# Kernel tuning notes

Measured on AMD Instinct MI355X. Metric: run time of the kernel, lower is better.

## Reference

```python
import jax, jax.numpy as jnp
import numpy as np

D = 2048
N_HEAD = 16
D_HEAD = D // N_HEAD
EXP = 4
EPS = 1e-6


def setup_inputs() -> dict:
    key = jax.random.key(0)
    ks = jax.random.split(key, 8)
    b, s = 2, 2048
    scale = 0.02
    return {
        "x": jax.random.normal(ks[0], (b, s, D), dtype=jnp.float32),
        "w_qkv": jax.random.normal(ks[1], (D, 3 * D), dtype=jnp.float32) * scale,
        "w_o": jax.random.normal(ks[2], (D, D), dtype=jnp.float32) * scale,
        "w_up": jax.random.normal(ks[3], (D, EXP * D), dtype=jnp.float32) * scale,
        "w_gate": jax.random.normal(ks[4], (D, EXP * D), dtype=jnp.float32) * scale,
        "w_down": jax.random.normal(ks[5], (EXP * D, D), dtype=jnp.float32) * scale,
        "scale1": jnp.ones((D,), dtype=jnp.float32),
        "scale2": jnp.ones((D,), dtype=jnp.float32),
    }


def _rmsnorm(x, scale):
    rms = jnp.sqrt(jnp.mean(x * x, axis=-1, keepdims=True) + EPS)
    return x / rms * scale


def _attention(x, w_qkv, w_o):
    b, s, d = x.shape
    qkv = x @ w_qkv  # [b, s, 3d]
    q, k, v = jnp.split(qkv, 3, axis=-1)
    # [b, h, s, dh]
    q = q.reshape(b, s, N_HEAD, D_HEAD).transpose(0, 2, 1, 3)
    k = k.reshape(b, s, N_HEAD, D_HEAD).transpose(0, 2, 1, 3)
    v = v.reshape(b, s, N_HEAD, D_HEAD).transpose(0, 2, 1, 3)
    scores = jnp.einsum("bhqd,bhkd->bhqk", q, k) / np.sqrt(D_HEAD).astype(np.float32)
    causal = jnp.tril(jnp.ones((s, s), dtype=bool))
    scores = jnp.where(causal, scores, -jnp.inf)
    attn = jax.nn.softmax(scores, axis=-1)
    out = jnp.einsum("bhqk,bhkd->bhqd", attn, v)
    out = out.transpose(0, 2, 1, 3).reshape(b, s, d)
    return out @ w_o


def _mlp(x, w_up, w_gate, w_down):
    return (x @ w_up * jax.nn.silu(x @ w_gate)) @ w_down


def reference(x, w_qkv, w_o, w_up, w_gate, w_down, scale1, scale2):
    x = x + _attention(_rmsnorm(x, scale1), w_qkv, w_o)
    x = x + _mlp(_rmsnorm(x, scale2), w_up, w_gate, w_down)
    return x
```

## Files before the change

### kernel.cpp

```cpp
#include <hip/hip_runtime.h>

typedef unsigned short u16;
typedef __bf16 bfrag8 __attribute__((ext_vector_type(8)));
typedef float f32x4 __attribute__((ext_vector_type(4)));

#define MFMA16(a, b, c) __builtin_amdgcn_mfma_f32_16x16x32_bf16((a), (b), (c), 0, 0, 0)

static __device__ __forceinline__ u16 bf_bits(float f) {
  unsigned int u = __builtin_bit_cast(unsigned int, f);
  unsigned int r = (u + 0x7fffu + ((u >> 16) & 1u)) >> 16;
  return (u16)r;
}
static __device__ __forceinline__ float f_from_bits(u16 u) {
  unsigned int w = ((unsigned int)u) << 16;
  return __builtin_bit_cast(float, w);
}
static __device__ __forceinline__ void gload16(const void* g, void* l) {
  __builtin_amdgcn_global_load_lds(
      (const __attribute__((address_space(1))) void*)g,
      (__attribute__((address_space(3))) void*)l, 16, 0, 0);
}

__global__ __launch_bounds__(256) void k_transpose_bf16(const float* __restrict__ src,
                                                        u16* __restrict__ dst,
                                                        int K, int N) {
  __shared__ float tile[32][33];
  const int n0 = blockIdx.x * 32;
  const int k0 = blockIdx.y * 32;
  const int t = threadIdx.x;
  const int lr = t >> 5;
  const int lc = t & 31;
#pragma unroll
  for (int i = 0; i < 4; ++i)
    tile[lr + i * 8][lc] = src[(size_t)(k0 + lr + i * 8) * N + n0 + lc];
  __syncthreads();
#pragma unroll
  for (int i = 0; i < 4; ++i)
    dst[(size_t)(n0 + lr + i * 8) * K + k0 + lc] = bf_bits(tile[lc][lr + i * 8]);
}

__global__ __launch_bounds__(256) void k_transpose_v(const u16* __restrict__ qkv,
                                                     u16* __restrict__ vtg) {
  __shared__ u16 tile[32][33];
  const int bh = blockIdx.z, b = bh >> 4, hh = bh & 15;
  const int s0 = blockIdx.x * 32, d0 = blockIdx.y * 32;
  const int t = threadIdx.x;
  const int lr = t >> 5, lc = t & 31;
#pragma unroll
  for (int i = 0; i < 4; ++i)
    tile[lr + i * 8][lc] =
        qkv[(size_t)(b * 2048 + s0 + lr + i * 8) * 6144 + 4096 + hh * 128 + d0 + lc];
  __syncthreads();
#pragma unroll
  for (int i = 0; i < 4; ++i)
    vtg[(size_t)bh * 128 * 2048 + (size_t)(d0 + lr + i * 8) * 2048 + s0 + lc] =
        tile[lc][lr + i * 8];
}

__global__ __launch_bounds__(256) void k_rmsnorm(const float* __restrict__ x,
                                                 const float* __restrict__ sc,
                                                 u16* __restrict__ o) {
  const int row = blockIdx.x;
  const int t = threadIdx.x;
  const float4* x4 = (const float4*)(x + (size_t)row * 2048);
  float4 a = x4[t];
  float4 b = x4[t + 256];
  float ss = a.x * a.x + a.y * a.y + a.z * a.z + a.w * a.w +
             b.x * b.x + b.y * b.y + b.z * b.z + b.w * b.w;
#pragma unroll
  for (int off = 32; off > 0; off >>= 1) ss += __shfl_down(ss, off);
  __shared__ float red[4];
  if ((t & 63) == 0) red[t >> 6] = ss;
  __syncthreads();
  const float inv = rsqrtf((red[0] + red[1] + red[2] + red[3]) * (1.0f / 2048.0f) + 1e-6f);
  const float4* s4 = (const float4*)sc;
  float4 sa = s4[t], sb = s4[t + 256];
  ushort4 pa, pb;
  pa.x = bf_bits(a.x * inv * sa.x); pa.y = bf_bits(a.y * inv * sa.y);
  pa.z = bf_bits(a.z * inv * sa.z); pa.w = bf_bits(a.w * inv * sa.w);
  pb.x = bf_bits(b.x * inv * sb.x); pb.y = bf_bits(b.y * inv * sb.y);
  pb.z = bf_bits(b.z * inv * sb.z); pb.w = bf_bits(b.w * inv * sb.w);
  *(ushort4*)(o + (size_t)row * 2048 + t * 4) = pa;
  *(ushort4*)(o + (size_t)row * 2048 + (t + 256) * 4) = pb;
}

template <int EPI, int K, int PART>
__global__ __launch_bounds__(256, 4) void k_gemm(const u16* __restrict__ A,
                                                 const u16* __restrict__ Bt,
                                                 int M, int N,
                                                 float* __restrict__ outF,
                                                 u16* __restrict__ outB,
                                                 const float* __restrict__ resid,
                                                 const u16* __restrict__ gate) {
  __shared__ u16 sm[16384];
  char* smC = (char*)sm;
  const int nbx = gridDim.x;
  const int f = blockIdx.x + nbx * blockIdx.y;
  int m0, n0;
  if (PART == 0) {
    const int nsl = nbx >> 3;
    const int x = f & 7;
    const int j = f >> 3;
    n0 = (x * nsl + (j % nsl)) * 128;
    m0 = (j / nsl) * 128;
  } else {
    const int msl = (int)gridDim.y >> 3;
    const int x = f & 7;
    const int j = f >> 3;
    m0 = (x * msl + (j % msl)) * 128;
    n0 = (j / msl) * 128;
  }

  const int t = threadIdx.x;
  const int wid = t >> 6, lane = t & 63;
  const int wm = wid >> 1, wn = wid & 1;
  const int l15 = lane & 15, lhi = lane >> 4;
  const int lhi16 = lhi * 16;
  const int swz = (l15 & 7) << 4;

  f32x4 acc[4][4];
#pragma unroll
  for (int i = 0; i < 4; ++i)
#pragma unroll
    for (int j2 = 0; j2 < 4; ++j2) acc[i][j2] = (f32x4){0.f, 0.f, 0.f, 0.f};

  const int sr = lane >> 3;
  const int csw = (((lane & 7) * 16) ^ (sr << 4)) >> 1;
  const u16* Asrc = A + (size_t)(m0 + wid * 32 + sr) * K + csw;
  const u16* Bsrc = Bt + (size_t)(n0 + wid * 32 + sr) * K + csw;
  char* adst = smC + wid * 4096 + lane * 16;
  char* bdst = smC + 16384 + wid * 4096 + lane * 16;

  for (int kt = 0; kt < K / 64; ++kt) {
    __syncthreads();
    const u16* as = Asrc + kt * 64;
    const u16* bs = Bsrc + kt * 64;
#pragma unroll
    for (int c = 0; c < 4; ++c) {
      gload16(as + (size_t)c * 8 * K, adst + c * 1024);
      gload16(bs + (size_t)c * 8 * K, bdst + c * 1024);
    }
    asm volatile("s_waitcnt vmcnt(0)" ::: "memory");
    __syncthreads();

#pragma unroll
    for (int kh = 0; kh < 2; ++kh) {
      const int ko = kh * 64 + lhi16;
      bfrag8 a0 = *(const bfrag8*)(smC + (wm * 64 + 0 * 16 + l15) * 128 + (ko ^ swz));
      bfrag8 a1 = *(const bfrag8*)(smC + (wm * 64 + 1 * 16 + l15) * 128 + (ko ^ swz));
      bfrag8 a2 = *(const bfrag8*)(smC + (wm * 64 + 2 * 16 + l15) * 128 + (ko ^ swz));
      bfrag8 a3 = *(const bfrag8*)(smC + (wm * 64 + 3 * 16 + l15) * 128 + (ko ^ swz));
      bfrag8 b0 = *(const bfrag8*)(smC + 16384 + (wn * 64 + 0 * 16 + l15) * 128 + (ko ^ swz));
      bfrag8 b1 = *(const bfrag8*)(smC + 16384 + (wn * 64 + 1 * 16 + l15) * 128 + (ko ^ swz));
      bfrag8 b2 = *(const bfrag8*)(smC + 16384 + (wn * 64 + 2 * 16 + l15) * 128 + (ko ^ swz));
      bfrag8 b3 = *(const bfrag8*)(smC + 16384 + (wn * 64 + 3 * 16 + l15) * 128 + (ko ^ swz));
      acc[0][0] = MFMA16(a0, b0, acc[0][0]); acc[0][1] = MFMA16(a0, b1, acc[0][1]);
      acc[0][2] = MFMA16(a0, b2, acc[0][2]); acc[0][3] = MFMA16(a0, b3, acc[0][3]);
      acc[1][0] = MFMA16(a1, b0, acc[1][0]); acc[1][1] = MFMA16(a1, b1, acc[1][1]);
      acc[1][2] = MFMA16(a1, b2, acc[1][2]); acc[1][3] = MFMA16(a1, b3, acc[1][3]);
      acc[2][0] = MFMA16(a2, b0, acc[2][0]); acc[2][1] = MFMA16(a2, b1, acc[2][1]);
      acc[2][2] = MFMA16(a2, b2, acc[2][2]); acc[2][3] = MFMA16(a2, b3, acc[2][3]);
      acc[3][0] = MFMA16(a3, b0, acc[3][0]); acc[3][1] = MFMA16(a3, b1, acc[3][1]);
      acc[3][2] = MFMA16(a3, b2, acc[3][2]); acc[3][3] = MFMA16(a3, b3, acc[3][3]);
    }
  }

#pragma unroll
  for (int i = 0; i < 4; ++i) {
#pragma unroll
    for (int j2 = 0; j2 < 4; ++j2) {
      const int mr = m0 + wm * 64 + i * 16 + lhi * 4;
      const int nc = n0 + wn * 64 + j2 * 16 + l15;
#pragma unroll
      for (int r = 0; r < 4; ++r) {
        const size_t idx = (size_t)(mr + r) * N + nc;
        const float v = acc[i][j2][r];
        if (EPI == 0) {
          outB[idx] = bf_bits(v);
        } else if (EPI == 1) {
          outF[idx] = resid[idx] + v;
        } else {
          float g = f_from_bits(gate[idx]);
          float s = g / (1.f + __expf(-g));
          outB[idx] = bf_bits(v * s);
        }
      }
    }
  }
}

template <int EPI, int K, int PART>
__global__ __launch_bounds__(256, 3) void k_gemm2(const u16* __restrict__ A,
                                                  const u16* __restrict__ Bt,
                                                  int N,
                                                  float* __restrict__ outF,
                                                  u16* __restrict__ outB,
                                                  const float* __restrict__ resid) {
  __shared__ u16 sm[24576];
  char* smC = (char*)sm;
  const int nbx = gridDim.x;
  const int f = blockIdx.x + nbx * blockIdx.y;
  int m0, np;
  if (PART == 0) {
    const int nsl = nbx >> 3;
    const int x = f & 7;
    const int j = f >> 3;
    np = x * nsl + (j % nsl);
    m0 = (j / nsl) * 128;
  } else {
    const int msl = (int)gridDim.y >> 3;
    const int x = f & 7;
    const int j = f >> 3;
    m0 = (x * msl + (j % msl)) * 128;
    np = j / msl;
  }
  const int n0 = np * 256;

  const int t = threadIdx.x;
  const int wid = t >> 6, lane = t & 63;
  const int wm = wid >> 1, wn = wid & 1;
  const int l15 = lane & 15, lhi = lane >> 4;
  const int lhi16 = lhi * 16;
  const int swz = (l15 & 7) << 4;

  f32x4 acc0[4][4], acc1[4][4];
#pragma unroll
  for (int i = 0; i < 4; ++i)
#pragma unroll
    for (int j2 = 0; j2 < 4; ++j2) {
      acc0[i][j2] = (f32x4){0.f, 0.f, 0.f, 0.f};
      acc1[i][j2] = (f32x4){0.f, 0.f, 0.f, 0.f};
    }

  const int sr = lane >> 3;
  const int csw = (((lane & 7) * 16) ^ (sr << 4)) >> 1;
  const u16* Asrc = A + (size_t)(m0 + wid * 32 + sr) * K + csw;
  const u16* B0src = Bt + (size_t)(n0 + wid * 32 + sr) * K + csw;
  const u16* B1src = Bt + (size_t)(n0 + 128 + wid * 32 + sr) * K + csw;
  char* adst = smC + wid * 4096 + lane * 16;
  char* b0dst = smC + 16384 + wid * 4096 + lane * 16;
  char* b1dst = smC + 32768 + wid * 4096 + lane * 16;

  for (int kt = 0; kt < K / 64; ++kt) {
    __syncthreads();
    const u16* as = Asrc + kt * 64;
    const u16* b0s = B0src + kt * 64;
    const u16* b1s = B1src + kt * 64;
#pragma unroll
    for (int c = 0; c < 4; ++c) {
      gload16(as + (size_t)c * 8 * K, adst + c * 1024);
      gload16(b0s + (size_t)c * 8 * K, b0dst + c * 1024);
      gload16(b1s + (size_t)c * 8 * K, b1dst + c * 1024);
    }
    asm volatile("s_waitcnt vmcnt(0)" ::: "memory");
    __syncthreads();

#pragma unroll
    for (int kh = 0; kh < 2; ++kh) {
      const int ko = (kh * 64 + lhi16);
      bfrag8 a0 = *(const bfrag8*)(smC + (wm * 64 + 0 * 16 + l15) * 128 + (ko ^ swz));
      bfrag8 a1 = *(const bfrag8*)(smC + (wm * 64 + 1 * 16 + l15) * 128 + (ko ^ swz));
      bfrag8 a2 = *(const bfrag8*)(smC + (wm * 64 + 2 * 16 + l15) * 128 + (ko ^ swz));
      bfrag8 a3 = *(const bfrag8*)(smC + (wm * 64 + 3 * 16 + l15) * 128 + (ko ^ swz));
      bfrag8 g0 = *(const bfrag8*)(smC + 16384 + (wn * 64 + 0 * 16 + l15) * 128 + (ko ^ swz));
      bfrag8 g1 = *(const bfrag8*)(smC + 16384 + (wn * 64 + 1 * 16 + l15) * 128 + (ko ^ swz));
      bfrag8 g2 = *(const bfrag8*)(smC + 16384 + (wn * 64 + 2 * 16 + l15) * 128 + (ko ^ swz));
      bfrag8 g3 = *(const bfrag8*)(smC + 16384 + (wn * 64 + 3 * 16 + l15) * 128 + (ko ^ swz));
      acc0[0][0] = MFMA16(a0, g0, acc0[0][0]); acc0[0][1] = MFMA16(a0, g1, acc0[0][1]);
      acc0[0][2] = MFMA16(a0, g2, acc0[0][2]); acc0[0][3] = MFMA16(a0, g3, acc0[0][3]);
      acc0[1][0] = MFMA16(a1, g0, acc0[1][0]); acc0[1][1] = MFMA16(a1, g1, acc0[1][1]);
      acc0[1][2] = MFMA16(a1, g2, acc0[1][2]); acc0[1][3] = MFMA16(a1, g3, acc0[1][3]);
      acc0[2][0] = MFMA16(a2, g0, acc0[2][0]); acc0[2][1] = MFMA16(a2, g1, acc0[2][1]);
      acc0[2][2] = MFMA16(a2, g2, acc0[2][2]); acc0[2][3] = MFMA16(a2, g3, acc0[2][3]);
      acc0[3][0] = MFMA16(a3, g0, acc0[3][0]); acc0[3][1] = MFMA16(a3, g1, acc0[3][1]);
      acc0[3][2] = MFMA16(a3, g2, acc0[3][2]); acc0[3][3] = MFMA16(a3, g3, acc0[3][3]);
      bfrag8 u0 = *(const bfrag8*)(smC + 32768 + (wn * 64 + 0 * 16 + l15) * 128 + (ko ^ swz));
      bfrag8 u1 = *(const bfrag8*)(smC + 32768 + (wn * 64 + 1 * 16 + l15) * 128 + (ko ^ swz));
      bfrag8 u2 = *(const bfrag8*)(smC + 32768 + (wn * 64 + 2 * 16 + l15) * 128 + (ko ^ swz));
      bfrag8 u3 = *(const bfrag8*)(smC + 32768 + (wn * 64 + 3 * 16 + l15) * 128 + (ko ^ swz));
      acc1[0][0] = MFMA16(a0, u0, acc1[0][0]); acc1[0][1] = MFMA16(a0, u1, acc1[0][1]);
      acc1[0][2] = MFMA16(a0, u2, acc1[0][2]); acc1[0][3] = MFMA16(a0, u3, acc1[0][3]);
      acc1[1][0] = MFMA16(a1, u0, acc1[1][0]); acc1[1][1] = MFMA16(a1, u1, acc1[1][1]);
      acc1[1][2] = MFMA16(a1, u2, acc1[1][2]); acc1[1][3] = MFMA16(a1, u3, acc1[1][3]);
      acc1[2][0] = MFMA16(a2, u0, acc1[2][0]); acc1[2][1] = MFMA16(a2, u1, acc1[2][1]);
      acc1[2][2] = MFMA16(a2, u2, acc1[2][2]); acc1[2][3] = MFMA16(a2, u3, acc1[2][3]);
      acc1[3][0] = MFMA16(a3, u0, acc1[3][0]); acc1[3][1] = MFMA16(a3, u1, acc1[3][1]);
      acc1[3][2] = MFMA16(a3, u2, acc1[3][2]); acc1[3][3] = MFMA16(a3, u3, acc1[3][3]);
    }
  }

#pragma unroll
  for (int h = 0; h < 2; ++h) {
#pragma unroll
    for (int i = 0; i < 4; ++i) {
#pragma unroll
      for (int j2 = 0; j2 < 4; ++j2) {
        const int mr = m0 + wm * 64 + i * 16 + lhi * 4;
        const int nc = n0 + h * 128 + wn * 64 + j2 * 16 + l15;
#pragma unroll
        for (int r = 0; r < 4; ++r) {
          const size_t idx = (size_t)(mr + r) * N + nc;
          const float v = h ? acc1[i][j2][r] : acc0[i][j2][r];
          if (EPI == 0) {
            outB[idx] = bf_bits(v);
          } else {
            outF[idx] = resid[idx] + v;
          }
        }
      }
    }
  }
}

template <int K>
__global__ __launch_bounds__(256, 3) void k_gemm_mlp(const u16* __restrict__ A,
                                                     const u16* __restrict__ Bg,
                                                     const u16* __restrict__ Bu,
                                                     int N,
                                                     u16* __restrict__ outB) {
  __shared__ u16 sm[24576];
  char* smC = (char*)sm;
  const int nbx = gridDim.x;
  const int f = blockIdx.x + nbx * blockIdx.y;
  const int nsl = nbx >> 3;
  const int x = f & 7;
  const int j = f >> 3;
  const int n0 = (x * nsl + (j % nsl)) * 128;
  const int m0 = (j / nsl) * 128;

  const int t = threadIdx.x;
  const int wid = t >> 6, lane = t & 63;
  const int wm = wid >> 1, wn = wid & 1;
  const int l15 = lane & 15, lhi = lane >> 4;
  const int lhi16 = lhi * 16;
  const int swz = (l15 & 7) << 4;

  f32x4 accg[4][4], accu[4][4];
#pragma unroll
  for (int i = 0; i < 4; ++i)
#pragma unroll
    for (int j2 = 0; j2 < 4; ++j2) {
      accg[i][j2] = (f32x4){0.f, 0.f, 0.f, 0.f};
      accu[i][j2] = (f32x4){0.f, 0.f, 0.f, 0.f};
    }

  const int sr = lane >> 3;
  const int csw = (((lane & 7) * 16) ^ (sr << 4)) >> 1;
  const u16* Asrc = A + (size_t)(m0 + wid * 32 + sr) * K + csw;
  const u16* Bgsrc = Bg + (size_t)(n0 + wid * 32 + sr) * K + csw;
  const u16* Busrc = Bu + (size_t)(n0 + wid * 32 + sr) * K + csw;
  char* adst = smC + wid * 4096 + lane * 16;
  char* bgdst = smC + 16384 + wid * 4096 + lane * 16;
  char* budst = smC + 32768 + wid * 4096 + lane * 16;

  for (int kt = 0; kt < K / 64; ++kt) {
    __syncthreads();
    const u16* as = Asrc + kt * 64;
    const u16* gs = Bgsrc + kt * 64;
    const u16* us = Busrc + kt * 64;
#pragma unroll
    for (int c = 0; c < 4; ++c) {
      gload16(as + (size_t)c * 8 * K, adst + c * 1024);
      gload16(gs + (size_t)c * 8 * K, bgdst + c * 1024);
      gload16(us + (size_t)c * 8 * K, budst + c * 1024);
    }
    asm volatile("s_waitcnt vmcnt(0)" ::: "memory");
    __syncthreads();

#pragma unroll
    for (int kh = 0; kh < 2; ++kh) {
      const int ko = (kh * 64 + lhi16);
      bfrag8 a0 = *(const bfrag8*)(smC + (wm * 64 + 0 * 16 + l15) * 128 + (ko ^ swz));
      bfrag8 a1 = *(const bfrag8*)(smC + (wm * 64 + 1 * 16 + l15) * 128 + (ko ^ swz));
      bfrag8 a2 = *(const bfrag8*)(smC + (wm * 64 + 2 * 16 + l15) * 128 + (ko ^ swz));
      bfrag8 a3 = *(const bfrag8*)(smC + (wm * 64 + 3 * 16 + l15) * 128 + (ko ^ swz));
      bfrag8 g0 = *(const bfrag8*)(smC + 16384 + (wn * 64 + 0 * 16 + l15) * 128 + (ko ^ swz));
      bfrag8 g1 = *(const bfrag8*)(smC + 16384 + (wn * 64 + 1 * 16 + l15) * 128 + (ko ^ swz));
      bfrag8 g2 = *(const bfrag8*)(smC + 16384 + (wn * 64 + 2 * 16 + l15) * 128 + (ko ^ swz));
      bfrag8 g3 = *(const bfrag8*)(smC + 16384 + (wn * 64 + 3 * 16 + l15) * 128 + (ko ^ swz));
      accg[0][0] = MFMA16(a0, g0, accg[0][0]); accg[0][1] = MFMA16(a0, g1, accg[0][1]);
      accg[0][2] = MFMA16(a0, g2, accg[0][2]); accg[0][3] = MFMA16(a0, g3, accg[0][3]);
      accg[1][0] = MFMA16(a1, g0, accg[1][0]); accg[1][1] = MFMA16(a1, g1, accg[1][1]);
      accg[1][2] = MFMA16(a1, g2, accg[1][2]); accg[1][3] = MFMA16(a1, g3, accg[1][3]);
      accg[2][0] = MFMA16(a2, g0, accg[2][0]); accg[2][1] = MFMA16(a2, g1, accg[2][1]);
      accg[2][2] = MFMA16(a2, g2, accg[2][2]); accg[2][3] = MFMA16(a2, g3, accg[2][3]);
      accg[3][0] = MFMA16(a3, g0, accg[3][0]); accg[3][1] = MFMA16(a3, g1, accg[3][1]);
      accg[3][2] = MFMA16(a3, g2, accg[3][2]); accg[3][3] = MFMA16(a3, g3, accg[3][3]);
      bfrag8 u0 = *(const bfrag8*)(smC + 32768 + (wn * 64 + 0 * 16 + l15) * 128 + (ko ^ swz));
      bfrag8 u1 = *(const bfrag8*)(smC + 32768 + (wn * 64 + 1 * 16 + l15) * 128 + (ko ^ swz));
      bfrag8 u2 = *(const bfrag8*)(smC + 32768 + (wn * 64 + 2 * 16 + l15) * 128 + (ko ^ swz));
      bfrag8 u3 = *(const bfrag8*)(smC + 32768 + (wn * 64 + 3 * 16 + l15) * 128 + (ko ^ swz));
      accu[0][0] = MFMA16(a0, u0, accu[0][0]); accu[0][1] = MFMA16(a0, u1, accu[0][1]);
      accu[0][2] = MFMA16(a0, u2, accu[0][2]); accu[0][3] = MFMA16(a0, u3, accu[0][3]);
      accu[1][0] = MFMA16(a1, u0, accu[1][0]); accu[1][1] = MFMA16(a1, u1, accu[1][1]);
      accu[1][2] = MFMA16(a1, u2, accu[1][2]); accu[1][3] = MFMA16(a1, u3, accu[1][3]);
      accu[2][0] = MFMA16(a2, u0, accu[2][0]); accu[2][1] = MFMA16(a2, u1, accu[2][1]);
      accu[2][2] = MFMA16(a2, u2, accu[2][2]); accu[2][3] = MFMA16(a2, u3, accu[2][3]);
      accu[3][0] = MFMA16(a3, u0, accu[3][0]); accu[3][1] = MFMA16(a3, u1, accu[3][1]);
      accu[3][2] = MFMA16(a3, u2, accu[3][2]); accu[3][3] = MFMA16(a3, u3, accu[3][3]);
    }
  }

#pragma unroll
  for (int i = 0; i < 4; ++i) {
#pragma unroll
    for (int j2 = 0; j2 < 4; ++j2) {
      const int mr = m0 + wm * 64 + i * 16 + lhi * 4;
      const int nc = n0 + wn * 64 + j2 * 16 + l15;
#pragma unroll
      for (int r = 0; r < 4; ++r) {
        const float g = accg[i][j2][r];
        const float u = accu[i][j2][r];
        const float s = g / (1.f + __expf(-g));
        outB[(size_t)(mr + r) * N + nc] = bf_bits(u * s);
      }
    }
  }
}

__global__ __launch_bounds__(512) void k_attn(const u16* __restrict__ qkv,
                                              const u16* __restrict__ vtg,
                                              u16* __restrict__ out) {
  const int S = 2048, LD = 6144;
  const float scale = 0.0883883476483184405f;
  const int fid = blockIdx.x;
  const int p = fid >> 1, s = fid & 1;
  const int bh = p & 31;
  const int pq = p >> 5;
  const int qt = s ? (15 - pq) : pq;
  const int b = bh >> 4, hh = bh & 15;
  const int t = threadIdx.x;
  const int wave = t >> 6, lane = t & 63;
  const int l15 = lane & 15, lhi = lane >> 4;
  const int lhi16 = lhi * 16;
  const int swz = (l15 & 7) << 4;

  __shared__ u16 Kt[64 * 128];
  __shared__ u16 Vt[128 * 64];
  __shared__ u16 Pl[8][16][72];
  char* KtC = (char*)Kt;
  char* VtC = (char*)Vt;

  const int qrow = qt * 128 + wave * 16 + l15;
  const size_t qoff = (size_t)(b * S + qrow) * LD + hh * 128 + lhi * 8;
  bfrag8 qf[4];
#pragma unroll
  for (int ks = 0; ks < 4; ++ks) qf[ks] = *(const bfrag8*)(qkv + qoff + ks * 32);

  f32x4 oacc[8];
#pragma unroll
  for (int j = 0; j < 8; ++j) oacc[j] = (f32x4){0.f, 0.f, 0.f, 0.f};
  float m_i[4], l_i[4];
#pragma unroll
  for (int r = 0; r < 4; ++r) { m_i[r] = -INFINITY; l_i[r] = 0.f; }

  const int q_my = qt * 128 + wave * 16 + lhi * 4;
  const int q_wave_last = qt * 128 + wave * 16 + 15;

  const int keyA = t >> 4, keyB = 32 + (t >> 4);
  const int oK = (t & 15) * 16;
  const int dA = t >> 3, dB = 64 + (t >> 3);
  const int oV = (t & 7) * 16;
  const u16* kbase = qkv + (size_t)(b * S) * LD + 2048 + hh * 128;
  const u16* vbase = vtg + (size_t)bh * 128 * S;
  const u16* ksrcA = kbase + (size_t)keyA * LD + ((oK ^ ((keyA & 7) << 4)) >> 1);
  const u16* ksrcB = kbase + (size_t)keyB * LD + ((oK ^ ((keyB & 7) << 4)) >> 1);
  const u16* vsrcA = vbase + (size_t)dA * S + ((oV ^ ((dA & 7) << 4)) >> 1);
  const u16* vsrcB = vbase + (size_t)dB * S + ((oV ^ ((dB & 7) << 4)) >> 1);
  const unsigned int ldso0 = wave * 1024 + lane * 16;
  const unsigned int ldso1 = 8192 + wave * 1024 + lane * 16;
  const size_t kstep = (size_t)64 * LD;

  const int kt_max = 2 * qt + 1;
  for (int kt = 0; kt <= kt_max; ++kt) {
    __syncthreads();
    gload16(ksrcA + (size_t)kt * kstep, KtC + ldso0);
    gload16(ksrcB + (size_t)kt * kstep, KtC + ldso1);
    gload16(vsrcA + kt * 64, VtC + ldso0);
    gload16(vsrcB + kt * 64, VtC + ldso1);
    __syncthreads();

    if (kt * 64 <= q_wave_last) {
      f32x4 sfr[4];
#pragma unroll
      for (int j = 0; j < 4; ++j) {
        sfr[j] = (f32x4){0.f, 0.f, 0.f, 0.f};
        const int krow = j * 16 + l15;
#pragma unroll
        for (int ks = 0; ks < 4; ++ks) {
          bfrag8 kf = *(const bfrag8*)(KtC + krow * 256 + ((ks * 64 + lhi16) ^ swz));
          sfr[j] = MFMA16(qf[ks], kf, sfr[j]);
        }
      }
      float sv[4][4], rmax[4];
#pragma unroll
      for (int r = 0; r < 4; ++r) rmax[r] = -INFINITY;
#pragma unroll
      for (int j = 0; j < 4; ++j) {
        const int key = kt * 64 + j * 16 + l15;
#pragma unroll
        for (int r = 0; r < 4; ++r) {
          float v = sfr[j][r] * scale;
          v = (key <= q_my + r) ? v : -INFINITY;
          sv[j][r] = v;
          rmax[r] = fmaxf(rmax[r], v);
        }
      }
#pragma unroll
      for (int r = 0; r < 4; ++r) {
        float v = rmax[r];
        v = fmaxf(v, __shfl_xor(v, 1));
        v = fmaxf(v, __shfl_xor(v, 2));
        v = fmaxf(v, __shfl_xor(v, 4));
        v = fmaxf(v, __shfl_xor(v, 8));
        rmax[r] = v;
      }
      float alpha[4], rsum[4];
#pragma unroll
      for (int r = 0; r < 4; ++r) {
        float mn = fmaxf(m_i[r], rmax[r]);
        alpha[r] = __expf(m_i[r] - mn);
        m_i[r] = mn;
        rsum[r] = 0.f;
      }
#pragma unroll
      for (int j = 0; j < 4; ++j) {
#pragma unroll
        for (int r = 0; r < 4; ++r) {
          float p2 = __expf(sv[j][r] - m_i[r]);
          rsum[r] += p2;
          Pl[wave][lhi * 4 + r][j * 16 + l15] = bf_bits(p2);
        }
      }
#pragma unroll
      for (int r = 0; r < 4; ++r) {
        float v = rsum[r];
        v += __shfl_xor(v, 1); v += __shfl_xor(v, 2);
        v += __shfl_xor(v, 4); v += __shfl_xor(v, 8);
        l_i[r] = l_i[r] * alpha[r] + v;
      }
#pragma unroll
      for (int j = 0; j < 8; ++j)
#pragma unroll
        for (int r = 0; r < 4; ++r) oacc[j][r] *= alpha[r];

#pragma unroll
      for (int ks2 = 0; ks2 < 2; ++ks2) {
        bfrag8 pf = *(const bfrag8*)&Pl[wave][l15][ks2 * 32 + lhi * 8];
#pragma unroll
        for (int j = 0; j < 8; ++j) {
          const int d = j * 16 + l15;
          bfrag8 vf = *(const bfrag8*)(VtC + d * 128 + ((ks2 * 64 + lhi16) ^ swz));
          oacc[j] = MFMA16(pf, vf, oacc[j]);
        }
      }
    }
  }

#pragma unroll
  for (int r = 0; r < 4; ++r) {
    const float inv = 1.f / l_i[r];
    const size_t tok = (size_t)b * S + qt * 128 + wave * 16 + lhi * 4 + r;
#pragma unroll
    for (int j = 0; j < 8; ++j)
      out[tok * 2048 + hh * 128 + j * 16 + l15] = bf_bits(oacc[j][r] * inv);
  }
}

extern "C" void kernel_launch(void* const* d_in, const int* in_sizes, int n_in,
                              void* d_out, int out_size, void* d_ws, size_t ws_size,
                              hipStream_t stream) {
  (void)in_sizes; (void)n_in; (void)out_size; (void)ws_size;
  const float* x      = (const float*)d_in[0];
  const float* w_qkv  = (const float*)d_in[1];
  const float* w_o    = (const float*)d_in[2];
  const float* w_up   = (const float*)d_in[3];
  const float* w_gate = (const float*)d_in[4];
  const float* w_down = (const float*)d_in[5];
  const float* scale1 = (const float*)d_in[6];
  const float* scale2 = (const float*)d_in[7];
  float* out = (float*)d_out;

  u16* B       = (u16*)d_ws;
  u16* wqkvT   = B;
  u16* woT     = wqkvT  + (size_t)6144 * 2048;
  u16* wgateT  = woT    + (size_t)2048 * 2048;
  u16* wupT    = wgateT + (size_t)8192 * 2048;
  u16* wdownT  = wupT   + (size_t)8192 * 2048;
  u16* xn      = wdownT + (size_t)2048 * 8192;
  u16* qkvb    = xn     + (size_t)4096 * 2048;
  u16* attnb   = qkvb   + (size_t)4096 * 6144;
  float* y1    = (float*)(attnb + (size_t)4096 * 2048);
  u16* vtg     = (u16*)y1;
  u16* hbuf    = qkvb;

  dim3 blk(256);
  k_transpose_bf16<<<dim3(192, 64), blk, 0, stream>>>(w_qkv,  wqkvT,  2048, 6144);
  k_transpose_bf16<<<dim3(64, 64),  blk, 0, stream>>>(w_o,    woT,    2048, 2048);
  k_transpose_bf16<<<dim3(256, 64), blk, 0, stream>>>(w_gate, wgateT, 2048, 8192);
  k_transpose_bf16<<<dim3(256, 64), blk, 0, stream>>>(w_up,   wupT,   2048, 8192);
  k_transpose_bf16<<<dim3(64, 256), blk, 0, stream>>>(w_down, wdownT, 8192, 2048);

  k_rmsnorm<<<4096, blk, 0, stream>>>(x, scale1, xn);
  k_gemm2<0, 2048, 0><<<dim3(24, 32), blk, 0, stream>>>(xn, wqkvT, 6144, nullptr, qkvb, nullptr);
  k_transpose_v<<<dim3(64, 4, 32), blk, 0, stream>>>(qkvb, vtg);
  k_attn<<<dim3(512), dim3(512), 0, stream>>>(qkvb, vtg, attnb);
  k_gemm<1, 2048, 1><<<dim3(16, 32), blk, 0, stream>>>(attnb, woT, 4096, 2048, y1, nullptr, x, nullptr);
  k_rmsnorm<<<4096, blk, 0, stream>>>(y1, scale2, xn);
  k_gemm_mlp<2048><<<dim3(64, 32), blk, 0, stream>>>(xn, wgateT, wupT, 8192, hbuf);
  k_gemm<1, 8192, 1><<<dim3(16, 32), blk, 0, stream>>>(hbuf, wdownT, 4096, 2048, out, nullptr, y1, nullptr);
}
```

Before: 817.8 us.

## Split-K the down projection GEMM into two halves with a combine kernel

```diff
diff --git a/kernel.cpp b/kernel.cpp
--- a/kernel.cpp
+++ b/kernel.cpp
@@ -82,6 +82,17 @@
   pb.z = bf_bits(b.z * inv * sb.z); pb.w = bf_bits(b.w * inv * sb.w);
   *(ushort4*)(o + (size_t)row * 2048 + t * 4) = pa;
   *(ushort4*)(o + (size_t)row * 2048 + (t + 256) * 4) = pb;
+}
+
+__global__ __launch_bounds__(256) void k_combine(float* __restrict__ out,
+                                                 const float* __restrict__ part0,
+                                                 const float* __restrict__ resid) {
+  const size_t i = ((size_t)blockIdx.x * 256 + threadIdx.x) * 4;
+  float4 o = *(const float4*)(out + i);
+  float4 p = *(const float4*)(part0 + i);
+  float4 r = *(const float4*)(resid + i);
+  o.x += p.x + r.x; o.y += p.y + r.y; o.z += p.z + r.z; o.w += p.w + r.w;
+  *(float4*)(out + i) = o;
 }
 
 template <int EPI, int K, int PART>
@@ -189,17 +200,19 @@
   }
 }
 
-template <int EPI, int K, int PART>
+template <int EPI, int K, int KLEN, int PART>
 __global__ __launch_bounds__(256, 3) void k_gemm2(const u16* __restrict__ A,
                                                   const u16* __restrict__ Bt,
                                                   int N,
                                                   float* __restrict__ outF,
                                                   u16* __restrict__ outB,
-                                                  const float* __restrict__ resid) {
+                                                  const float* __restrict__ resid,
+                                                  float* __restrict__ outF2) {
   __shared__ u16 sm[24576];
   char* smC = (char*)sm;
   const int nbx = gridDim.x;
   const int f = blockIdx.x + nbx * blockIdx.y;
+  const int z = blockIdx.z;
   int m0, np;
   if (PART == 0) {
     const int nsl = nbx >> 3;
@@ -215,6 +228,7 @@
     np = j / msl;
   }
   const int n0 = np * 256;
+  const int koff = z * KLEN;
 
   const int t = threadIdx.x;
   const int wid = t >> 6, lane = t & 63;
@@ -234,14 +248,14 @@
 
   const int sr = lane >> 3;
   const int csw = (((lane & 7) * 16) ^ (sr << 4)) >> 1;
-  const u16* Asrc = A + (size_t)(m0 + wid * 32 + sr) * K + csw;
-  const u16* B0src = Bt + (size_t)(n0 + wid * 32 + sr) * K + csw;
-  const u16* B1src = Bt + (size_t)(n0 + 128 + wid * 32 + sr) * K + csw;
+  const u16* Asrc = A + (size_t)(m0 + wid * 32 + sr) * K + csw + koff;
+  const u16* B0src = Bt + (size_t)(n0 + wid * 32 + sr) * K + csw + koff;
+  const u16* B1src = Bt + (size_t)(n0 + 128 + wid * 32 + sr) * K + csw + koff;
   char* adst = smC + wid * 4096 + lane * 16;
   char* b0dst = smC + 16384 + wid * 4096 + lane * 16;
   char* b1dst = smC + 32768 + wid * 4096 + lane * 16;
 
-  for (int kt = 0; kt < K / 64; ++kt) {
+  for (int kt = 0; kt < KLEN / 64; ++kt) {
     __syncthreads();
     const u16* as = Asrc + kt * 64;
     const u16* b0s = B0src + kt * 64;
@@ -289,6 +303,7 @@
     }
   }
 
+  float* wout = (EPI == 2 && blockIdx.z == 1) ? outF2 : outF;
 #pragma unroll
   for (int h = 0; h < 2; ++h) {
 #pragma unroll
@@ -303,8 +318,10 @@
           const float v = h ? acc1[i][j2][r] : acc0[i][j2][r];
           if (EPI == 0) {
             outB[idx] = bf_bits(v);
+          } else if (EPI == 1) {
+            outF[idx] = resid[idx] + v;
           } else {
-            outF[idx] = resid[idx] + v;
+            wout[idx] = v;
           }
         }
       }
@@ -593,6 +610,7 @@
   float* y1    = (float*)(attnb + (size_t)4096 * 2048);
   u16* vtg     = (u16*)y1;
   u16* hbuf    = qkvb;
+  float* part0 = (float*)wqkvT;
 
   dim3 blk(256);
   k_transpose_bf16<<<dim3(192, 64), blk, 0, stream>>>(w_qkv,  wqkvT,  2048, 6144);
@@ -602,11 +620,12 @@
   k_transpose_bf16<<<dim3(64, 256), blk, 0, stream>>>(w_down, wdownT, 8192, 2048);
 
   k_rmsnorm<<<4096, blk, 0, stream>>>(x, scale1, xn);
-  k_gemm2<0, 2048, 0><<<dim3(24, 32), blk, 0, stream>>>(xn, wqkvT, 6144, nullptr, qkvb, nullptr);
+  k_gemm2<0, 2048, 2048, 0><<<dim3(24, 32), blk, 0, stream>>>(xn, wqkvT, 6144, nullptr, qkvb, nullptr, nullptr);
   k_transpose_v<<<dim3(64, 4, 32), blk, 0, stream>>>(qkvb, vtg);
   k_attn<<<dim3(512), dim3(512), 0, stream>>>(qkvb, vtg, attnb);
   k_gemm<1, 2048, 1><<<dim3(16, 32), blk, 0, stream>>>(attnb, woT, 4096, 2048, y1, nullptr, x, nullptr);
   k_rmsnorm<<<4096, blk, 0, stream>>>(y1, scale2, xn);
   k_gemm_mlp<2048><<<dim3(64, 32), blk, 0, stream>>>(xn, wgateT, wupT, 8192, hbuf);
-  k_gemm<1, 8192, 1><<<dim3(16, 32), blk, 0, stream>>>(hbuf, wdownT, 4096, 2048, out, nullptr, y1, nullptr);
-}
+  k_gemm2<2, 8192, 4096, 1><<<dim3(8, 32, 2), blk, 0, stream>>>(hbuf, wdownT, 2048, part0, nullptr, nullptr, out);
+  k_combine<<<8192, blk, 0, stream>>>(out, part0, y1);
+}
```

Result: no change. 831.3 us (+1.7%).

## Split down-projection GEMM three ways along K with wider tiles and combine pass

Applied to the files above, without the earlier changes.

```diff
diff --git a/kernel.cpp b/kernel.cpp
--- a/kernel.cpp
+++ b/kernel.cpp
@@ -82,6 +82,20 @@
   pb.z = bf_bits(b.z * inv * sb.z); pb.w = bf_bits(b.w * inv * sb.w);
   *(ushort4*)(o + (size_t)row * 2048 + t * 4) = pa;
   *(ushort4*)(o + (size_t)row * 2048 + (t + 256) * 4) = pb;
+}
+
+__global__ __launch_bounds__(256) void k_combine3(float* __restrict__ out,
+                                                  const float* __restrict__ p0,
+                                                  const float* __restrict__ p1,
+                                                  const float* __restrict__ resid) {
+  const size_t i = ((size_t)blockIdx.x * 256 + threadIdx.x) * 4;
+  float4 o = *(const float4*)(out + i);
+  float4 a = *(const float4*)(p0 + i);
+  float4 b = *(const float4*)(p1 + i);
+  float4 r = *(const float4*)(resid + i);
+  o.x += a.x + b.x + r.x; o.y += a.y + b.y + r.y;
+  o.z += a.z + b.z + r.z; o.w += a.w + b.w + r.w;
+  *(float4*)(out + i) = o;
 }
 
 template <int EPI, int K, int PART>
@@ -313,6 +327,119 @@
 }
 
 template <int K>
+__global__ __launch_bounds__(256, 3) void k_gemm2s(const u16* __restrict__ A,
+                                                   const u16* __restrict__ Bt,
+                                                   int N,
+                                                   float* __restrict__ p0,
+                                                   float* __restrict__ p1,
+                                                   float* __restrict__ p2) {
+  __shared__ u16 sm[24576];
+  char* smC = (char*)sm;
+  const int nbx = gridDim.x;
+  const int f = blockIdx.x + nbx * blockIdx.y;
+  const int z = blockIdx.z;
+  const int msl = (int)gridDim.y >> 3;
+  const int x = f & 7;
+  const int j = f >> 3;
+  const int m0 = (x * msl + (j % msl)) * 128;
+  const int np = j / msl;
+  const int n0 = np * 256;
+  const int koff = z * 2752;
+  const int ktn = (z == 2) ? 42 : 43;
+
+  const int t = threadIdx.x;
+  const int wid = t >> 6, lane = t & 63;
+  const int wm = wid >> 1, wn = wid & 1;
+  const int l15 = lane & 15, lhi = lane >> 4;
+  const int lhi16 = lhi * 16;
+  const int swz = (l15 & 7) << 4;
+
+  f32x4 acc0[4][4], acc1[4][4];
+#pragma unroll
+  for (int i = 0; i < 4; ++i)
+#pragma unroll
+    for (int j2 = 0; j2 < 4; ++j2) {
+      acc0[i][j2] = (f32x4){0.f, 0.f, 0.f, 0.f};
+      acc1[i][j2] = (f32x4){0.f, 0.f, 0.f, 0.f};
+    }
+
+  const int sr = lane >> 3;
+  const int csw = (((lane & 7) * 16) ^ (sr << 4)) >> 1;
+  const u16* Asrc = A + (size_t)(m0 + wid * 32 + sr) * K + csw + koff;
+  const u16* B0src = Bt + (size_t)(n0 + wid * 32 + sr) * K + csw + koff;
+  const u16* B1src = Bt + (size_t)(n0 + 128 + wid * 32 + sr) * K + csw + koff;
+  char* adst = smC + wid * 4096 + lane * 16;
+  char* b0dst = smC + 16384 + wid * 4096 + lane * 16;
+  char* b1dst = smC + 32768 + wid * 4096 + lane * 16;
+
+  for (int kt = 0; kt < ktn; ++kt) {
+    __syncthreads();
+    const u16* as = Asrc + kt * 64;
+    const u16* b0s = B0src + kt * 64;
+    const u16* b1s = B1src + kt * 64;
+#pragma unroll
+    for (int c = 0; c < 4; ++c) {
+      gload16(as + (size_t)c * 8 * K, adst + c * 1024);
+      gload16(b0s + (size_t)c * 8 * K, b0dst + c * 1024);
+      gload16(b1s + (size_t)c * 8 * K, b1dst + c * 1024);
+    }
+    asm volatile("s_waitcnt vmcnt(0)" ::: "memory");
+    __syncthreads();
+
+#pragma unroll
+    for (int kh = 0; kh < 2; ++kh) {
+      const int ko = (kh * 64 + lhi16);
+      bfrag8 a0 = *(const bfrag8*)(smC + (wm * 64 + 0 * 16 + l15) * 128 + (ko ^ swz));
+      bfrag8 a1 = *(const bfrag8*)(smC + (wm * 64 + 1 * 16 + l15) * 128 + (ko ^ swz));
+      bfrag8 a2 = *(const bfrag8*)(smC + (wm * 64 + 2 * 16 + l15) * 128 + (ko ^ swz));
+      bfrag8 a3 = *(const bfrag8*)(smC + (wm * 64 + 3 * 16 + l15) * 128 + (ko ^ swz));
+      bfrag8 g0 = *(const bfrag8*)(smC + 16384 + (wn * 64 + 0 * 16 + l15) * 128 + (ko ^ swz));
+      bfrag8 g1 = *(const bfrag8*)(smC + 16384 + (wn * 64 + 1 * 16 + l15) * 128 + (ko ^ swz));
+      bfrag8 g2 = *(const bfrag8*)(smC + 16384 + (wn * 64 + 2 * 16 + l15) * 128 + (ko ^ swz));
+      bfrag8 g3 = *(const bfrag8*)(smC + 16384 + (wn * 64 + 3 * 16 + l15) * 128 + (ko ^ swz));
+      acc0[0][0] = MFMA16(a0, g0, acc0[0][0]); acc0[0][1] = MFMA16(a0, g1, acc0[0][1]);
+      acc0[0][2] = MFMA16(a0, g2, acc0[0][2]); acc0[0][3] = MFMA16(a0, g3, acc0[0][3]);
+      acc0[1][0] = MFMA16(a1, g0, acc0[1][0]); acc0[1][1] = MFMA16(a1, g1, acc0[1][1]);
+      acc0[1][2] = MFMA16(a1, g2, acc0[1][2]); acc0[1][3] = MFMA16(a1, g3, acc0[1][3]);
+      acc0[2][0] = MFMA16(a2, g0, acc0[2][0]); acc0[2][1] = MFMA16(a2, g1, acc0[2][1]);
+      acc0[2][2] = MFMA16(a2, g2, acc0[2][2]); acc0[2][3] = MFMA16(a2, g3, acc0[2][3]);
+      acc0[3][0] = MFMA16(a3, g0, acc0[3][0]); acc0[3][1] = MFMA16(a3, g1, acc0[3][1]);
+      acc0[3][2] = MFMA16(a3, g2, acc0[3][2]); acc0[3][3] = MFMA16(a3, g3, acc0[3][3]);
+      bfrag8 u0 = *(const bfrag8*)(smC + 32768 + (wn * 64 + 0 * 16 + l15) * 128 + (ko ^ swz));
+      bfrag8 u1 = *(const bfrag8*)(smC + 32768 + (wn * 64 + 1 * 16 + l15) * 128 + (ko ^ swz));
+      bfrag8 u2 = *(const bfrag8*)(smC + 32768 + (wn * 64 + 2 * 16 + l15) * 128 + (ko ^ swz));
+      bfrag8 u3 = *(const bfrag8*)(smC + 32768 + (wn * 64 + 3 * 16 + l15) * 128 + (ko ^ swz));
+      acc1[0][0] = MFMA16(a0, u0, acc1[0][0]); acc1[0][1] = MFMA16(a0, u1, acc1[0][1]);
+      acc1[0][2] = MFMA16(a0, u2, acc1[0][2]); acc1[0][3] = MFMA16(a0, u3, acc1[0][3]);
+      acc1[1][0] = MFMA16(a1, u0, acc1[1][0]); acc1[1][1] = MFMA16(a1, u1, acc1[1][1]);
+      acc1[1][2] = MFMA16(a1, u2, acc1[1][2]); acc1[1][3] = MFMA16(a1, u3, acc1[1][3]);
+      acc1[2][0] = MFMA16(a2, u0, acc1[2][0]); acc1[2][1] = MFMA16(a2, u1, acc1[2][1]);
+      acc1[2][2] = MFMA16(a2, u2, acc1[2][2]); acc1[2][3] = MFMA16(a2, u3, acc1[2][3]);
+      acc1[3][0] = MFMA16(a3, u0, acc1[3][0]); acc1[3][1] = MFMA16(a3, u1, acc1[3][1]);
+      acc1[3][2] = MFMA16(a3, u2, acc1[3][2]); acc1[3][3] = MFMA16(a3, u3, acc1[3][3]);
+    }
+  }
+
+  float* wout = (z == 0) ? p0 : ((z == 1) ? p1 : p2);
+#pragma unroll
+  for (int h = 0; h < 2; ++h) {
+#pragma unroll
+    for (int i = 0; i < 4; ++i) {
+#pragma unroll
+      for (int j2 = 0; j2 < 4; ++j2) {
+        const int mr = m0 + wm * 64 + i * 16 + lhi * 4;
+        const int nc = n0 + h * 128 + wn * 64 + j2 * 16 + l15;
+#pragma unroll
+        for (int r = 0; r < 4; ++r) {
+          const size_t idx = (size_t)(mr + r) * N + nc;
+          wout[idx] = h ? acc1[i][j2][r] : acc0[i][j2][r];
+        }
+      }
+    }
+  }
+}
+
+template <int K>
 __global__ __launch_bounds__(256, 3) void k_gemm_mlp(const u16* __restrict__ A,
                                                      const u16* __restrict__ Bg,
                                                      const u16* __restrict__ Bu,
@@ -593,6 +720,8 @@
   float* y1    = (float*)(attnb + (size_t)4096 * 2048);
   u16* vtg     = (u16*)y1;
   u16* hbuf    = qkvb;
+  float* part0 = (float*)wqkvT;
+  float* part1 = (float*)wgateT;
 
   dim3 blk(256);
   k_transpose_bf16<<<dim3(192, 64), blk, 0, stream>>>(w_qkv,  wqkvT,  2048, 6144);
@@ -608,5 +737,6 @@
   k_gemm<1, 2048, 1><<<dim3(16, 32), blk, 0, stream>>>(attnb, woT, 4096, 2048, y1, nullptr, x, nullptr);
   k_rmsnorm<<<4096, blk, 0, stream>>>(y1, scale2, xn);
   k_gemm_mlp<2048><<<dim3(64, 32), blk, 0, stream>>>(xn, wgateT, wupT, 8192, hbuf);
-  k_gemm<1, 8192, 1><<<dim3(16, 32), blk, 0, stream>>>(hbuf, wdownT, 4096, 2048, out, nullptr, y1, nullptr);
-}
+  k_gemm2s<8192><<<dim3(8, 32, 3), blk, 0, stream>>>(hbuf, wdownT, 2048, part0, part1, out);
+  k_combine3<<<8192, blk, 0, stream>>>(out, part0, part1, y1);
+}
```

Measured after the change: 816.2 us. Within noise of the previous version (-0.2%).
